# Kernel tuning notes

Measured on AMD Instinct MI355X. Metric: run time of the kernel, lower is better.

## Reference

```python
import jax, jax.numpy as jnp
import numpy as np

B, OBS, H, N = 16384, 512, 1024, 9

def setup_inputs() -> dict:
    key = jax.random.key(0)
    ks = jax.random.split(key, 12)
    s = 0.02
    return {
        "obs": jax.random.normal(ks[0], (B, OBS), jnp.float32),
        "agent_positions": jax.random.normal(ks[1], (B, N, 3), jnp.float32),
        "W1": jax.random.normal(ks[2], (OBS, H), jnp.float32) * s,
        "b1": jnp.zeros((H,), jnp.float32),
        "W2": jax.random.normal(ks[3], (H, H), jnp.float32) * s,
        "b2": jnp.zeros((H,), jnp.float32),
        "Wc1": jax.random.normal(ks[4], (H, H // 2), jnp.float32) * s,
        "bc1": jnp.zeros((H // 2,), jnp.float32),
        "Wc2": jax.random.normal(ks[5], (H // 2, 1), jnp.float32) * s,
        "bc2": jnp.zeros((1,), jnp.float32),
        "Wt1": jax.random.normal(ks[6], (H, H // 2), jnp.float32) * s,
        "bt1": jnp.zeros((H // 2,), jnp.float32),
        "Wt2": jax.random.normal(ks[7], (H // 2, 1), jnp.float32) * s,
        "bt2": jnp.zeros((1,), jnp.float32),
        "Wk1": jax.random.normal(ks[8], (2 * H, H), jnp.float32) * s,
        "bk1": jnp.zeros((H,), jnp.float32),
        "Wk2": jax.random.normal(ks[9], (H, 1), jnp.float32) * s,
        "bk2": jnp.zeros((1,), jnp.float32),
    }


def reference(obs, agent_positions, W1, b1, W2, b2, Wc1, bc1, Wc2, bc2,
              Wt1, bt1, Wt2, bt2, Wk1, bk1, Wk2, bk2):
    # global features: Linear->ReLU->Linear->ReLU
    g = jax.nn.relu(obs @ W1 + b1)
    g = jax.nn.relu(g @ W2 + b2)  # [B, H]

    # Each per-agent head is applied to the SAME g in the original loop,
    # so one pass + broadcast is mathematically identical.
    cov = jax.nn.sigmoid(jax.nn.relu(g @ Wc1 + bc1) @ Wc2 + bc2)  # [B,1]
    trk = jax.nn.sigmoid(jax.nn.relu(g @ Wt1 + bt1) @ Wt2 + bt2)  # [B,1]
    coop_in = jnp.concatenate([g, g], axis=-1)                    # [B,2H]
    coop = jax.nn.sigmoid(jax.nn.relu(coop_in @ Wk1 + bk1) @ Wk2 + bk2)  # [B,1]
    # mean over 8 identical cooperation scores == the score itself

    coverage = jnp.broadcast_to(cov, (cov.shape[0], N))      # [B, N]
    tracking = jnp.broadcast_to(trk, (trk.shape[0], N))      # [B, N]
    cooperation = jnp.broadcast_to(coop, (coop.shape[0], N)) # [B, N]
    return (coverage, tracking, cooperation)
```

## Files before the change

### kernel.cpp

```cpp
#include <hip/hip_runtime.h>
#include <hip/hip_bf16.h>

#define B_ROWS 16384
#define OBS_D  512
#define H_D    1024
#define N_AG   9

typedef __attribute__((ext_vector_type(8))) short short8;
typedef __attribute__((ext_vector_type(4))) float floatx4;

__device__ __forceinline__ unsigned short f_to_bf_raw(float f) {
  union { float f; unsigned u; } c; c.f = f;
  unsigned u = c.u;
  u = u + 0x7FFF + ((u >> 16) & 1);
  return (unsigned short)(u >> 16);
}

__device__ __forceinline__ size_t frag_off(int n, int k, int KT32) {
  const int ft = (n >> 4) * KT32 + (k >> 5);
  const int ln = (n & 15) | (((k >> 3) & 3) << 4);
  return ((size_t)ft * 64 + ln) * 8 + (k & 7);
}

__global__ __launch_bounds__(256) void prep_all(
    const float* __restrict__ obs,
    const float* __restrict__ W1, const float* __restrict__ W2,
    const float* __restrict__ Wc1, const float* __restrict__ Wt1,
    const float* __restrict__ Wk1,
    const float* __restrict__ bc1, const float* __restrict__ bt1,
    const float* __restrict__ bk1,
    const float* __restrict__ Wc2, const float* __restrict__ Wt2,
    const float* __restrict__ Wk2,
    unsigned short* __restrict__ obs_bf,
    unsigned short* __restrict__ W1f, unsigned short* __restrict__ W2f,
    unsigned short* __restrict__ WHf,
    float* __restrict__ bias2048, float* __restrict__ w2cat) {
  __shared__ float t[32][33];
  const int bx  = blockIdx.x;
  const int tid = threadIdx.x;

  if (bx < 4096) {
    int i = (bx * 256 + tid) * 8;
    float4 a = *(const float4*)(obs + i);
    float4 b = *(const float4*)(obs + i + 4);
    short8 o;
    o[0] = (short)f_to_bf_raw(a.x); o[1] = (short)f_to_bf_raw(a.y);
    o[2] = (short)f_to_bf_raw(a.z); o[3] = (short)f_to_bf_raw(a.w);
    o[4] = (short)f_to_bf_raw(b.x); o[5] = (short)f_to_bf_raw(b.y);
    o[6] = (short)f_to_bf_raw(b.z); o[7] = (short)f_to_bf_raw(b.w);
    *(short8*)(obs_bf + i) = o;
    return;
  }

  const int tx = tid & 31;
  const int ty = tid >> 5;

  if (bx < 4608) {
    const int tt = bx - 4096;
    const int k0 = (tt & 15) * 32;
    const int n0 = (tt >> 4) * 32;
#pragma unroll
    for (int i = ty; i < 32; i += 8)
      t[i][tx] = W1[(size_t)(k0 + i) * 1024 + n0 + tx];
    __syncthreads();
#pragma unroll
    for (int i = ty; i < 32; i += 8)
      W1f[frag_off(n0 + i, k0 + tx, 16)] = f_to_bf_raw(t[tx][i]);
    return;
  }

  if (bx < 5632) {
    const int tt = bx - 4608;
    const int k0 = (tt & 31) * 32;
    const int n0 = (tt >> 5) * 32;
#pragma unroll
    for (int i = ty; i < 32; i += 8)
      t[i][tx] = W2[(size_t)(k0 + i) * 1024 + n0 + tx];
    __syncthreads();
#pragma unroll
    for (int i = ty; i < 32; i += 8)
      W2f[frag_off(n0 + i, k0 + tx, 32)] = f_to_bf_raw(t[tx][i]);
    return;
  }

  if (bx < 7680) {
    const int tt = bx - 5632;
    const int k0 = (tt & 31) * 32;
    const int n0 = (tt >> 5) * 32;
#pragma unroll
    for (int i = ty; i < 32; i += 8) {
      const int n = n0 + tx;
      float v;
      if (n0 < 512)
        v = Wc1[(size_t)(k0 + i) * 512 + n];
      else if (n0 < 1024)
        v = Wt1[(size_t)(k0 + i) * 512 + (n - 512)];
      else
        v = Wk1[(size_t)(k0 + i) * 1024 + (n - 1024)]
          + Wk1[(size_t)(k0 + i + 1024) * 1024 + (n - 1024)];
      t[i][tx] = v;
    }
    __syncthreads();
#pragma unroll
    for (int i = ty; i < 32; i += 8)
      WHf[frag_off(n0 + i, k0 + tx, 32)] = f_to_bf_raw(t[tx][i]);
    return;
  }

  {
    int n = (bx - 7680) * 256 + tid;
    float b, w;
    if (n < 512)       { b = bc1[n];        w = Wc2[n]; }
    else if (n < 1024) { b = bt1[n - 512];  w = Wt2[n - 512]; }
    else               { b = bk1[n - 1024]; w = Wk2[n - 1024]; }
    bias2048[n] = b;
    w2cat[n] = w;
  }
}

#define GLD_LDS(gp, lp)                                                        \
  __builtin_amdgcn_global_load_lds(                                            \
      (const __attribute__((address_space(1))) void*)(gp),                     \
      (__attribute__((address_space(3))) void*)(lp), 16, 0, 0)

#define GEMM_CORE_V9(ACC_DECL)                                                 \
  __shared__ __align__(16) unsigned short As[3][128 * 64];          \
  const int tid  = threadIdx.x;                                                \
  const int lane = tid & 63;                                                   \
  const int wave = tid >> 6;                                                   \
  const int m0 = blockIdx.x * 128;                                             \
  const int n0 = blockIdx.y * 128;                                             \
  const int wm = (wave & 1) * 64;                                              \
  const int wn = (wave >> 1) * 64;                                             \
  const int fr = lane & 15;                                                    \
  const int fq = lane >> 4;                                                    \
  ACC_DECL;                                                                    \
  constexpr int KT   = K >> 6;                      \
  constexpr int KT32 = K >> 5;                      \
  const size_t rowb = (size_t)K * 2;                                           \
  const int srow8  = lane >> 3;                   \
  const int schunk = (lane & 7) ^ srow8;          \
  const char* gA = (const char*)A + (size_t)(m0 + wave * 32 + srow8) * rowb    \
                   + schunk * 16;                                              \
  char* lA = (char*)&As[0][0] + wave * 4096 + lane * 16;                       \
  const unsigned short* gB =                                                   \
      Bf + ((size_t)(((n0 + wn) >> 4) * KT32) * 64 + lane) * 8;                \
  const int fsA = (wm + fr) * 128;                                             \
  const int sl0 = ((fq)     ^ (fr & 7)) * 16;                                  \
  const int sl1 = ((4 + fq) ^ (fr & 7)) * 16;                                  \
  short8 FbP[2][2][4];                                                         \
                  \
  _Pragma("unroll")                                                            \
  for (int j = 0; j < 4; ++j)                                                  \
    GLD_LDS(gA + (size_t)j * 8 * rowb, lA + j * 1024);                         \
  _Pragma("unroll")                                                            \
  for (int j = 0; j < 4; ++j)                                                  \
    GLD_LDS(gA + 128 + (size_t)j * 8 * rowb,                                   \
            (char*)&As[1][0] + wave * 4096 + lane * 16 + j * 1024);            \
  _Pragma("unroll")                                                            \
  for (int s = 0; s < 2; ++s)                                                  \
    _Pragma("unroll")                                                          \
    for (int ni = 0; ni < 4; ++ni)                                             \
      FbP[0][s][ni] = *(const short8*)(gB + ((size_t)ni * KT32 + s) * 512);    \
  _Pragma("unroll")                                                            \
  for (int k = 0; k < KT; ++k) {           \
    __syncthreads();            \
    if (k + 2 < KT) {                                                          \
      char* d = (char*)&As[(k + 2) % 3][0] + wave * 4096 + lane * 16;          \
      const char* g = gA + (size_t)(k + 2) * 128;                              \
      _Pragma("unroll")                                                        \
      for (int j = 0; j < 4; ++j)                                              \
        GLD_LDS(g + (size_t)j * 8 * rowb, d + j * 1024);                       \
    }                                                                          \
    if (k + 1 < KT) {                                                          \
      _Pragma("unroll")                                                        \
      for (int s = 0; s < 2; ++s)                                              \
        _Pragma("unroll")                                                      \
        for (int ni = 0; ni < 4; ++ni)                                         \
          FbP[(k + 1) & 1][s][ni] = *(const short8*)                           \
              (gB + ((size_t)ni * KT32 + 2 * (k + 1) + s) * 512);              \
    }                                                                          \
    const char* bA = (const char*)&As[k % 3][0];                               \
    short8 Fa0[4], Fa1[4];                                                     \
    _Pragma("unroll")                                                          \
    for (int mi = 0; mi < 4; ++mi)                                             \
      Fa0[mi] = *(const short8*)(bA + fsA + mi * 2048 + sl0);                  \
    _Pragma("unroll")                                                          \
    for (int mi = 0; mi < 4; ++mi)                                             \
      Fa1[mi] = *(const short8*)(bA + fsA + mi * 2048 + sl1);                  \
    _Pragma("unroll")                                                          \
    for (int mi = 0; mi < 4; ++mi)                                             \
      _Pragma("unroll")                                                        \
      for (int ni = 0; ni < 4; ++ni)                                           \
        acc[mi][ni] = __builtin_amdgcn_mfma_f32_16x16x32_bf16(                 \
            Fa0[mi], FbP[k & 1][0][ni], acc[mi][ni], 0, 0, 0);                 \
    _Pragma("unroll")                                                          \
    for (int mi = 0; mi < 4; ++mi)                                             \
      _Pragma("unroll")                                                        \
      for (int ni = 0; ni < 4; ++ni)                                           \
        acc[mi][ni] = __builtin_amdgcn_mfma_f32_16x16x32_bf16(                 \
            Fa1[mi], FbP[k & 1][1][ni], acc[mi][ni], 0, 0, 0);                 \
  }

#define ACC_INIT                                                               \
  floatx4 acc[4][4];                                                           \
  _Pragma("unroll")                                                            \
  for (int i = 0; i < 4; ++i)                                                  \
    _Pragma("unroll")                                                          \
    for (int j = 0; j < 4; ++j) acc[i][j] = (floatx4){0.f, 0.f, 0.f, 0.f}

template <int K>
__global__ __launch_bounds__(256, 2) void gemm_bias_relu(
    const unsigned short* __restrict__ A,
    const unsigned short* __restrict__ Bf,
    const float* __restrict__ bias,
    unsigned short* __restrict__ C,
    int M, int N) {
  GEMM_CORE_V9(ACC_INIT)

#pragma unroll
  for (int ni = 0; ni < 4; ++ni) {
    const int gn = n0 + wn + ni * 16 + fr;
    const float bv = bias[gn];
#pragma unroll
    for (int mi = 0; mi < 4; ++mi) {
#pragma unroll
      for (int r = 0; r < 4; ++r) {
        const int gm = m0 + wm + mi * 16 + fq * 4 + r;
        float v = acc[mi][ni][r] + bv;
        v = v > 0.f ? v : 0.f;
        C[(size_t)gm * N + gn] = f_to_bf_raw(v);
      }
    }
  }
}

template <int K>
__global__ __launch_bounds__(256, 2) void gemm_heads_fused(
    const unsigned short* __restrict__ A,
    const unsigned short* __restrict__ Bf,
    const float* __restrict__ bias,
    const float* __restrict__ w2,
    float* __restrict__ part,
    int M, int N) {
  GEMM_CORE_V9(ACC_INIT)

  const int j = blockIdx.y * 2 + (wave >> 1);
  float w2v[4], bv[4];
#pragma unroll
  for (int ni = 0; ni < 4; ++ni) {
    const int gn = n0 + wn + ni * 16 + fr;
    w2v[ni] = w2[gn];
    bv[ni]  = bias[gn];
  }
#pragma unroll
  for (int mi = 0; mi < 4; ++mi) {
#pragma unroll
    for (int r = 0; r < 4; ++r) {
      float p = 0.f;
#pragma unroll
      for (int ni = 0; ni < 4; ++ni) {
        float v = acc[mi][ni][r] + bv[ni];
        v = v > 0.f ? v : 0.f;
        p += v * w2v[ni];
      }
      p += __shfl_xor(p, 1);
      p += __shfl_xor(p, 2);
      p += __shfl_xor(p, 4);
      p += __shfl_xor(p, 8);
      if (fr == 0) {
        const int gm = m0 + wm + mi * 16 + fq * 4 + r;
        part[(size_t)j * B_ROWS + gm] = p;
      }
    }
  }
}

__global__ __launch_bounds__(256) void final_out(
    const float* __restrict__ part,
    const float* __restrict__ bc2, const float* __restrict__ bt2,
    const float* __restrict__ bk2, float* __restrict__ out) {
  const int row = blockIdx.x * 256 + threadIdx.x;
  float sc = 0.f, st = 0.f, sk = 0.f;
#pragma unroll
  for (int j = 0; j < 8; ++j)  sc += part[(size_t)j * B_ROWS + row];
#pragma unroll
  for (int j = 8; j < 16; ++j) st += part[(size_t)j * B_ROWS + row];
#pragma unroll
  for (int j = 16; j < 32; ++j) sk += part[(size_t)j * B_ROWS + row];
  const float cv = 1.f / (1.f + expf(-(sc + bc2[0])));
  const float tv = 1.f / (1.f + expf(-(st + bt2[0])));
  const float kv = 1.f / (1.f + expf(-(sk + bk2[0])));
  float* o0 = out + (size_t)row * N_AG;
  float* o1 = out + (size_t)(B_ROWS + row) * N_AG;
  float* o2 = out + (size_t)(2 * B_ROWS + row) * N_AG;
#pragma unroll
  for (int a = 0; a < N_AG; ++a) { o0[a] = cv; o1[a] = tv; o2[a] = kv; }
}

extern "C" void kernel_launch(void* const* d_in, const int* in_sizes, int n_in,
                              void* d_out, int out_size, void* d_ws, size_t ws_size,
                              hipStream_t stream) {
  const float* obs = (const float*)d_in[0];
  const float* W1  = (const float*)d_in[2];
  const float* b1  = (const float*)d_in[3];
  const float* W2  = (const float*)d_in[4];
  const float* b2  = (const float*)d_in[5];
  const float* Wc1 = (const float*)d_in[6];
  const float* bc1 = (const float*)d_in[7];
  const float* Wc2 = (const float*)d_in[8];
  const float* bc2 = (const float*)d_in[9];
  const float* Wt1 = (const float*)d_in[10];
  const float* bt1 = (const float*)d_in[11];
  const float* Wt2 = (const float*)d_in[12];
  const float* bt2 = (const float*)d_in[13];
  const float* Wk1 = (const float*)d_in[14];
  const float* bk1 = (const float*)d_in[15];
  const float* Wk2 = (const float*)d_in[16];
  const float* bk2 = (const float*)d_in[17];
  float* out = (float*)d_out;

  char* ws = (char*)d_ws;
  const size_t MB = 1024 * 1024;
  const size_t FULL_NEED = 70 * MB + 16 * 1024;

  unsigned short *obs_bf, *W1f, *W2f, *WHf, *G1, *G;
  float *bias2048, *w2cat, *PART;
  const bool full = (ws_size == 0) || (ws_size >= FULL_NEED);

  if (full) {
    obs_bf   = (unsigned short*)(ws + 0);
    W1f      = (unsigned short*)(ws + 16 * MB);
    G        = (unsigned short*)(ws + 0);
    G1       = (unsigned short*)(ws + 32 * MB);
    PART     = (float*)(ws + 32 * MB);
    W2f      = (unsigned short*)(ws + 64 * MB);
    WHf      = (unsigned short*)(ws + 66 * MB);
    bias2048 = (float*)(ws + 70 * MB);
    w2cat    = (float*)(ws + 70 * MB + 8 * 1024);
  } else {
    obs_bf   = (unsigned short*)(ws + 0);
    G1       = (unsigned short*)(ws + 16 * MB);
    G        = (unsigned short*)(ws + 32 * MB);
    W1f      = (unsigned short*)(ws + 48 * MB);
    W2f      = (unsigned short*)(ws + 49 * MB);
    WHf      = (unsigned short*)(ws + 51 * MB);
    bias2048 = (float*)(ws + 55 * MB);
    w2cat    = (float*)(ws + 55 * MB + 8 * 1024);
    PART     = (float*)(ws + 55 * MB + 16 * 1024);
  }

  prep_all<<<7688, 256, 0, stream>>>(obs, W1, W2, Wc1, Wt1, Wk1,
                                     bc1, bt1, bk1, Wc2, Wt2, Wk2,
                                     obs_bf, W1f, W2f, WHf, bias2048, w2cat);

  if (full) {
    gemm_bias_relu<512><<<dim3(128, 8), 256, 0, stream>>>(
        obs_bf, W1f, b1, G1, B_ROWS, 1024);
    gemm_bias_relu<1024><<<dim3(128, 8), 256, 0, stream>>>(
        G1, W2f, b2, G, B_ROWS, 1024);
    gemm_heads_fused<1024><<<dim3(128, 16), 256, 0, stream>>>(
        G, WHf, bias2048, w2cat, PART, B_ROWS, 2048);
  } else {
    for (int h = 0; h < 2; ++h) {
      const size_t ro = (size_t)h * 8192;
      gemm_bias_relu<512><<<dim3(64, 8), 256, 0, stream>>>(
          obs_bf + ro * 512, W1f, b1, G1, 8192, 1024);
      gemm_bias_relu<1024><<<dim3(64, 8), 256, 0, stream>>>(
          G1, W2f, b2, G, 8192, 1024);
      gemm_heads_fused<1024><<<dim3(64, 16), 256, 0, stream>>>(
          G, WHf, bias2048, w2cat, PART + ro, 8192, 2048);
    }
  }

  final_out<<<B_ROWS / 256, 256, 0, stream>>>(PART, bc2, bt2, bk2, out);
}
```

Baseline: 246.6 us.

## Enlarge GEMM tiles to 256x256 with 8 waves and pinned barrier scheduling

Grows each GEMM block tile from 128x128 to 256x256, with 512 threads and each wave holding a 128x64 accumulator tile. This raises arithmetic intensity per loaded fragment. The K loop is restructured: A-fragment LDS reads and B-fragment global prefetches are interleaved with MFMA groups, split by sched_barrier-pinned s_barriers, with s_setprio raised around the MFMA bursts and explicit vmcnt/lgkmcnt waits replacing __syncthreads. The trade-offs are much higher register pressure (128 accumulator floats per lane) and a 96KB LDS triple buffer that limits occupancy. The grid also gets fewer blocks, which may hurt load balance across CUs.

```diff
diff --git a/kernel.cpp b/kernel.cpp
--- a/kernel.cpp
+++ b/kernel.cpp
@@ -123,14 +123,21 @@
       (const __attribute__((address_space(1))) void*)(gp),                     \
       (__attribute__((address_space(3))) void*)(lp), 16, 0, 0)
 
-#define GEMM_CORE_V9(ACC_DECL)                                                 \
-  __shared__ __align__(16) unsigned short As[3][128 * 64];          \
+#define SBAR_PINNED()                                                          \
+  __builtin_amdgcn_sched_barrier(0);                                           \
+  __builtin_amdgcn_s_barrier();                                                \
+  __builtin_amdgcn_sched_barrier(0)
+
+#define MFMA_BF16(a, b, c) __builtin_amdgcn_mfma_f32_16x16x32_bf16(a, b, c, 0, 0, 0)
+
+#define GEMM_CORE_V10(ACC_DECL)                                                \
+  __shared__ __align__(16) unsigned short As[3][256 * 64];          \
   const int tid  = threadIdx.x;                                                \
   const int lane = tid & 63;                                                   \
-  const int wave = tid >> 6;                                                   \
-  const int m0 = blockIdx.x * 128;                                             \
-  const int n0 = blockIdx.y * 128;                                             \
-  const int wm = (wave & 1) * 64;                                              \
+  const int wave = tid >> 6;                                         \
+  const int m0 = blockIdx.x * 256;                                             \
+  const int n0 = blockIdx.y * 256;                                             \
+  const int wm = (wave & 1) * 128;                  \
   const int wn = (wave >> 1) * 64;                                             \
   const int fr = lane & 15;                                                    \
   const int fq = lane >> 4;                                                    \
@@ -142,88 +149,98 @@
   const int schunk = (lane & 7) ^ srow8;          \
   const char* gA = (const char*)A + (size_t)(m0 + wave * 32 + srow8) * rowb    \
                    + schunk * 16;                                              \
-  char* lA = (char*)&As[0][0] + wave * 4096 + lane * 16;                       \
   const unsigned short* gB =                                                   \
       Bf + ((size_t)(((n0 + wn) >> 4) * KT32) * 64 + lane) * 8;                \
   const int fsA = (wm + fr) * 128;                                             \
   const int sl0 = ((fq)     ^ (fr & 7)) * 16;                                  \
   const int sl1 = ((4 + fq) ^ (fr & 7)) * 16;                                  \
   short8 FbP[2][2][4];                                                         \
-                  \
+        \
+        \
   _Pragma("unroll")                                                            \
   for (int j = 0; j < 4; ++j)                                                  \
-    GLD_LDS(gA + (size_t)j * 8 * rowb, lA + j * 1024);                         \
+    GLD_LDS(gA + (size_t)j * 8 * rowb,                                         \
+            (char*)&As[0][0] + wave * 4096 + lane * 16 + j * 1024);            \
+  __builtin_amdgcn_sched_barrier(0);                                           \
   _Pragma("unroll")                                                            \
   for (int j = 0; j < 4; ++j)                                                  \
     GLD_LDS(gA + 128 + (size_t)j * 8 * rowb,                                   \
             (char*)&As[1][0] + wave * 4096 + lane * 16 + j * 1024);            \
+  __builtin_amdgcn_sched_barrier(0);                                           \
   _Pragma("unroll")                                                            \
   for (int s = 0; s < 2; ++s)                                                  \
     _Pragma("unroll")                                                          \
     for (int ni = 0; ni < 4; ++ni)                                             \
       FbP[0][s][ni] = *(const short8*)(gB + ((size_t)ni * KT32 + s) * 512);    \
-  _Pragma("unroll")                                                            \
-  for (int k = 0; k < KT; ++k) {           \
-    __syncthreads();            \
-    if (k + 2 < KT) {                                                          \
-      char* d = (char*)&As[(k + 2) % 3][0] + wave * 4096 + lane * 16;          \
-      const char* g = gA + (size_t)(k + 2) * 128;                              \
+  __builtin_amdgcn_sched_barrier(0);                                           \
+  asm volatile("s_waitcnt vmcnt(12)" ::: "memory");        \
+  __builtin_amdgcn_s_barrier();                                                \
+  __builtin_amdgcn_sched_barrier(0);                                           \
+  _Pragma("unroll")                                                            \
+  for (int t = 0; t < KT; ++t) {           \
+    if (t + 2 < KT) {                      \
+      char* d = (char*)&As[(t + 2) % 3][0] + wave * 4096 + lane * 16;          \
+      const char* g = gA + (size_t)(t + 2) * 128;                              \
       _Pragma("unroll")                                                        \
       for (int j = 0; j < 4; ++j)                                              \
         GLD_LDS(g + (size_t)j * 8 * rowb, d + j * 1024);                       \
     }                                                                          \
-    if (k + 1 < KT) {                                                          \
+    const char* bA = (const char*)&As[t % 3][0];                               \
+    _Pragma("unroll")                                                          \
+    for (int p = 0; p < 4; ++p) {           \
+      short8 Fa00 = *(const short8*)(bA + fsA + (2 * p) * 2048     + sl0);     \
+      short8 Fa01 = *(const short8*)(bA + fsA + (2 * p) * 2048     + sl1);     \
+      short8 Fa10 = *(const short8*)(bA + fsA + (2 * p + 1) * 2048 + sl0);     \
+      short8 Fa11 = *(const short8*)(bA + fsA + (2 * p + 1) * 2048 + sl1);     \
+      if (t + 1 < KT) {                           \
+        FbP[(t + 1) & 1][0][p] = *(const short8*)                              \
+            (gB + ((size_t)p * KT32 + 2 * (t + 1)) * 512);                     \
+        FbP[(t + 1) & 1][1][p] = *(const short8*)                              \
+            (gB + ((size_t)p * KT32 + 2 * (t + 1) + 1) * 512);                 \
+      }                                                                        \
+      SBAR_PINNED();                                                           \
+      __builtin_amdgcn_s_setprio(1);                                           \
       _Pragma("unroll")                                                        \
-      for (int s = 0; s < 2; ++s)                                              \
-        _Pragma("unroll")                                                      \
-        for (int ni = 0; ni < 4; ++ni)                                         \
-          FbP[(k + 1) & 1][s][ni] = *(const short8*)                           \
-              (gB + ((size_t)ni * KT32 + 2 * (k + 1) + s) * 512);              \
+      for (int ni = 0; ni < 4; ++ni) {                                         \
+        acc[2 * p][ni]     = MFMA_BF16(Fa00, FbP[t & 1][0][ni], acc[2 * p][ni]);     \
+        acc[2 * p][ni]     = MFMA_BF16(Fa01, FbP[t & 1][1][ni], acc[2 * p][ni]);     \
+        acc[2 * p + 1][ni] = MFMA_BF16(Fa10, FbP[t & 1][0][ni], acc[2 * p + 1][ni]); \
+        acc[2 * p + 1][ni] = MFMA_BF16(Fa11, FbP[t & 1][1][ni], acc[2 * p + 1][ni]); \
+      }                                                                        \
+      __builtin_amdgcn_s_setprio(0);                                           \
+      if (p < 3) { SBAR_PINNED(); }                                            \
     }                                                                          \
-    const char* bA = (const char*)&As[k % 3][0];                               \
-    short8 Fa0[4], Fa1[4];                                                     \
-    _Pragma("unroll")                                                          \
-    for (int mi = 0; mi < 4; ++mi)                                             \
-      Fa0[mi] = *(const short8*)(bA + fsA + mi * 2048 + sl0);                  \
-    _Pragma("unroll")                                                          \
-    for (int mi = 0; mi < 4; ++mi)                                             \
-      Fa1[mi] = *(const short8*)(bA + fsA + mi * 2048 + sl1);                  \
-    _Pragma("unroll")                                                          \
-    for (int mi = 0; mi < 4; ++mi)                                             \
-      _Pragma("unroll")                                                        \
-      for (int ni = 0; ni < 4; ++ni)                                           \
-        acc[mi][ni] = __builtin_amdgcn_mfma_f32_16x16x32_bf16(                 \
-            Fa0[mi], FbP[k & 1][0][ni], acc[mi][ni], 0, 0, 0);                 \
-    _Pragma("unroll")                                                          \
-    for (int mi = 0; mi < 4; ++mi)                                             \
-      _Pragma("unroll")                                                        \
-      for (int ni = 0; ni < 4; ++ni)                                           \
-        acc[mi][ni] = __builtin_amdgcn_mfma_f32_16x16x32_bf16(                 \
-            Fa1[mi], FbP[k & 1][1][ni], acc[mi][ni], 0, 0, 0);                 \
+          \
+          \
+          \
+    __builtin_amdgcn_sched_barrier(0);                                         \
+    asm volatile("s_waitcnt vmcnt(12) lgkmcnt(0)" ::: "memory");               \
+    __builtin_amdgcn_s_barrier();                                              \
+    __builtin_amdgcn_sched_barrier(0);                                         \
   }
 
 #define ACC_INIT                                                               \
-  floatx4 acc[4][4];                                                           \
-  _Pragma("unroll")                                                            \
-  for (int i = 0; i < 4; ++i)                                                  \
+  floatx4 acc[8][4];                                                           \
+  _Pragma("unroll")                                                            \
+  for (int i = 0; i < 8; ++i)                                                  \
     _Pragma("unroll")                                                          \
     for (int j = 0; j < 4; ++j) acc[i][j] = (floatx4){0.f, 0.f, 0.f, 0.f}
 
 template <int K>
-__global__ __launch_bounds__(256, 2) void gemm_bias_relu(
+__global__ __launch_bounds__(512, 2) void gemm_bias_relu(
     const unsigned short* __restrict__ A,
     const unsigned short* __restrict__ Bf,
     const float* __restrict__ bias,
     unsigned short* __restrict__ C,
     int M, int N) {
-  GEMM_CORE_V9(ACC_INIT)
+  GEMM_CORE_V10(ACC_INIT)
 
 #pragma unroll
   for (int ni = 0; ni < 4; ++ni) {
     const int gn = n0 + wn + ni * 16 + fr;
     const float bv = bias[gn];
 #pragma unroll
-    for (int mi = 0; mi < 4; ++mi) {
+    for (int mi = 0; mi < 8; ++mi) {
 #pragma unroll
       for (int r = 0; r < 4; ++r) {
         const int gm = m0 + wm + mi * 16 + fq * 4 + r;
@@ -236,16 +253,16 @@
 }
 
 template <int K>
-__global__ __launch_bounds__(256, 2) void gemm_heads_fused(
+__global__ __launch_bounds__(512, 2) void gemm_heads_fused(
     const unsigned short* __restrict__ A,
     const unsigned short* __restrict__ Bf,
     const float* __restrict__ bias,
     const float* __restrict__ w2,
     float* __restrict__ part,
     int M, int N) {
-  GEMM_CORE_V9(ACC_INIT)
-
-  const int j = blockIdx.y * 2 + (wave >> 1);
+  GEMM_CORE_V10(ACC_INIT)
+
+  const int j = blockIdx.y * 4 + (wave >> 1);
   float w2v[4], bv[4];
 #pragma unroll
   for (int ni = 0; ni < 4; ++ni) {
@@ -254,7 +271,7 @@
     bv[ni]  = bias[gn];
   }
 #pragma unroll
-  for (int mi = 0; mi < 4; ++mi) {
+  for (int mi = 0; mi < 8; ++mi) {
 #pragma unroll
     for (int r = 0; r < 4; ++r) {
       float p = 0.f;
@@ -355,20 +372,20 @@
                                      obs_bf, W1f, W2f, WHf, bias2048, w2cat);
 
   if (full) {
-    gemm_bias_relu<512><<<dim3(128, 8), 256, 0, stream>>>(
+    gemm_bias_relu<512><<<dim3(64, 4), 512, 0, stream>>>(
         obs_bf, W1f, b1, G1, B_ROWS, 1024);
-    gemm_bias_relu<1024><<<dim3(128, 8), 256, 0, stream>>>(
+    gemm_bias_relu<1024><<<dim3(64, 4), 512, 0, stream>>>(
         G1, W2f, b2, G, B_ROWS, 1024);
-    gemm_heads_fused<1024><<<dim3(128, 16), 256, 0, stream>>>(
+    gemm_heads_fused<1024><<<dim3(64, 8), 512, 0, stream>>>(
         G, WHf, bias2048, w2cat, PART, B_ROWS, 2048);
   } else {
     for (int h = 0; h < 2; ++h) {
       const size_t ro = (size_t)h * 8192;
-      gemm_bias_relu<512><<<dim3(64, 8), 256, 0, stream>>>(
+      gemm_bias_relu<512><<<dim3(32, 4), 512, 0, stream>>>(
           obs_bf + ro * 512, W1f, b1, G1, 8192, 1024);
-      gemm_bias_relu<1024><<<dim3(64, 8), 256, 0, stream>>>(
+      gemm_bias_relu<1024><<<dim3(32, 4), 512, 0, stream>>>(
           G1, W2f, b2, G, 8192, 1024);
-      gemm_heads_fused<1024><<<dim3(64, 16), 256, 0, stream>>>(
+      gemm_heads_fused<1024><<<dim3(32, 8), 512, 0, stream>>>(
           G, WHf, bias2048, w2cat, PART + ro, 8192, 2048);
     }
   }
```

Result: slower. 262.1 us (+6.3%).

## Rewrite heads GEMM with 256x256 tiles, LDS-staged B, and explicit pipelining

Applied to the files above, without the earlier changes.

The fused heads GEMM moves to a new core with 256x256 block tiles and 512 threads (8 waves), each wave computing 128x64. Both A and B are now staged through a 128KB double-buffered LDS region using global_load_lds, and the loop uses explicit vmcnt waits, sched barriers and setprio around the MFMA bursts. The larger tile is meant to raise data reuse and cut global traffic on the biggest GEMM. The cost is more LDS per block (limiting occupancy) and more accumulator registers per wave.

```diff
diff --git a/kernel.cpp b/kernel.cpp
--- a/kernel.cpp
+++ b/kernel.cpp
@@ -122,6 +122,10 @@
   __builtin_amdgcn_global_load_lds(                                            \
       (const __attribute__((address_space(1))) void*)(gp),                     \
       (__attribute__((address_space(3))) void*)(lp), 16, 0, 0)
+
+#define SCB __builtin_amdgcn_sched_barrier(0)
+
+#define MFMA_BF16(a, b, c) __builtin_amdgcn_mfma_f32_16x16x32_bf16(a, b, c, 0, 0, 0)
 
 #define GEMM_CORE_V9(ACC_DECL)                                                 \
   __shared__ __align__(16) unsigned short As[3][128 * 64];          \
@@ -149,7 +153,6 @@
   const int sl0 = ((fq)     ^ (fr & 7)) * 16;                                  \
   const int sl1 = ((4 + fq) ^ (fr & 7)) * 16;                                  \
   short8 FbP[2][2][4];                                                         \
-                  \
   _Pragma("unroll")                                                            \
   for (int j = 0; j < 4; ++j)                                                  \
     GLD_LDS(gA + (size_t)j * 8 * rowb, lA + j * 1024);                         \
@@ -202,10 +205,112 @@
             Fa1[mi], FbP[k & 1][1][ni], acc[mi][ni], 0, 0, 0);                 \
   }
 
-#define ACC_INIT                                                               \
+#define ACC_INIT4                                                              \
   floatx4 acc[4][4];                                                           \
   _Pragma("unroll")                                                            \
   for (int i = 0; i < 4; ++i)                                                  \
+    _Pragma("unroll")                                                          \
+    for (int j = 0; j < 4; ++j) acc[i][j] = (floatx4){0.f, 0.f, 0.f, 0.f}
+
+#define ST_A16(T, kh)                                                          \
+  GLD_LDS(gA0 + (size_t)(T) * 128 + (kh) * 64,                                 \
+          Lds + ((T) & 1) * 65536 + (kh) * 16384 + lA0);                       \
+  GLD_LDS(gA1 + (size_t)(T) * 128 + (kh) * 64,                                 \
+          Lds + ((T) & 1) * 65536 + (kh) * 16384 + lA0 + 8192)
+
+#define ST_B16(T, kh)                                                          \
+  GLD_LDS(gB0 + (size_t)(2 * (T) + (kh)) * 1024,                               \
+          Lds + ((T) & 1) * 65536 + (kh) * 16384 + lB0);                       \
+  GLD_LDS(gB1 + (size_t)(2 * (T) + (kh)) * 1024,                               \
+          Lds + ((T) & 1) * 65536 + (kh) * 16384 + lB0 + 8192)
+
+#define ROW16(mi, FA)                                                          \
+  acc[mi][0] = MFMA_BF16(FA, Fb0v, acc[mi][0]);                                \
+  acc[mi][1] = MFMA_BF16(FA, Fb1v, acc[mi][1]);                                \
+  acc[mi][2] = MFMA_BF16(FA, Fb2v, acc[mi][2]);                                \
+  acc[mi][3] = MFMA_BF16(FA, Fb3v, acc[mi][3])
+
+#define PHASE16(TT, ks, STAGE_STMT, PRE_BAR2)                                  \
+  {                                                                            \
+    const char* pb = Lds + ((TT) & 1) * 65536 + (ks) * 16384;                  \
+    short8 Fa0 = *(const short8*)(pb + faB + 0 * 1024);                        \
+    short8 Fa1 = *(const short8*)(pb + faB + 1 * 1024);                        \
+    short8 Fa2 = *(const short8*)(pb + faB + 2 * 1024);                        \
+    short8 Fa3 = *(const short8*)(pb + faB + 3 * 1024);                        \
+    short8 Fa4 = *(const short8*)(pb + faB + 4 * 1024);                        \
+    short8 Fa5 = *(const short8*)(pb + faB + 5 * 1024);                        \
+    short8 Fa6 = *(const short8*)(pb + faB + 6 * 1024);                        \
+    short8 Fa7 = *(const short8*)(pb + faB + 7 * 1024);                        \
+    short8 Fb0v = *(const short8*)(pb + fbB);                                  \
+    short8 Fb1v = *(const short8*)(pb + fbB + 1024);                           \
+    short8 Fb2v = *(const short8*)(pb + fbB + 2048);                           \
+    short8 Fb3v = *(const short8*)(pb + fbB + 3072);                           \
+    STAGE_STMT;                                                                \
+    SCB; __builtin_amdgcn_s_barrier(); SCB;                                    \
+    __builtin_amdgcn_s_setprio(1);                                             \
+    ROW16(0, Fa0); ROW16(1, Fa1); ROW16(2, Fa2); ROW16(3, Fa3);                \
+    ROW16(4, Fa4); ROW16(5, Fa5); ROW16(6, Fa6); ROW16(7, Fa7);                \
+    __builtin_amdgcn_s_setprio(0);                                             \
+    PRE_BAR2;                                                                  \
+    SCB; __builtin_amdgcn_s_barrier(); SCB;                                    \
+  }
+
+#define GEMM_CORE_V16(ACC_DECL)                                                \
+  __shared__ __align__(16) char Lds[131072];                                   \
+  const int tid  = threadIdx.x;                                                \
+  const int lane = tid & 63;                                                   \
+  const int wave = tid >> 6;                                         \
+  const int m0 = blockIdx.x * 256;                                             \
+  const int n0 = blockIdx.y * 256;                                             \
+  const int wm = (wave & 1) * 128;                  \
+  const int wn = (wave >> 1) * 64;                                             \
+  const int fr = lane & 15;                                                    \
+  const int fq = lane >> 4;                                                    \
+  ACC_DECL;                                                                    \
+  constexpr int KT   = K >> 6;                                                 \
+  constexpr int KT32 = K >> 5;                                                 \
+  const size_t rowb = (size_t)K * 2;                                           \
+  const char* gA0 = (const char*)A                                             \
+      + (size_t)(m0 + wave * 16 + (lane >> 2)) * rowb                          \
+      + (((lane & 3) ^ ((lane >> 3) & 3)) * 16);                               \
+  const char* gA1 = gA0 + (size_t)128 * rowb;                                  \
+  const char* gB0 = (const char*)Bf                                            \
+      + ((size_t)((n0 >> 4) + wave) * KT32) * 1024 + lane * 16;                \
+  const char* gB1 = gB0 + (size_t)8 * KT32 * 1024;                             \
+  const int lA0 = wave * 1024 + lane * 16;                                     \
+  const int lB0 = 32768 + wave * 1024 + lane * 16;                             \
+  const int faB = (wm + fr) * 64 + ((fq ^ ((fr >> 1) & 3)) * 16);              \
+  const int fbB = 32768 + ((wave >> 1) * 4) * 1024 + lane * 16;                \
+               \
+  ST_A16(0, 0); ST_B16(0, 0); ST_A16(0, 1); ST_B16(0, 1);                      \
+  SCB;                                                                         \
+  ST_A16(1, 0); ST_B16(1, 0);                                                  \
+  SCB;                                                                         \
+  asm volatile("s_waitcnt vmcnt(4)" ::: "memory");       \
+  __builtin_amdgcn_s_barrier();                  \
+  SCB;                                                                         \
+  _Pragma("unroll")                                                            \
+  for (int T = 0; T < KT; ++T) {           \
+    PHASE16(T, 0,                                                              \
+            { if (T + 1 < KT) { ST_A16(T + 1, 1); ST_B16(T + 1, 1); } },       \
+            (void)0);                                                          \
+    PHASE16(T, 1,                                                              \
+            { if (T + 2 < KT) { ST_A16(T + 2, 0); ST_B16(T + 2, 0); } },       \
+            if (T + 1 < KT) {                                                  \
+              SCB;                                                             \
+              if (T + 2 < KT) {                                                \
+                asm volatile("s_waitcnt vmcnt(4)" ::: "memory");               \
+              } else {                                                         \
+                asm volatile("s_waitcnt vmcnt(0)" ::: "memory");               \
+              }                                                                \
+              SCB;                                                             \
+            });                                                                \
+  }
+
+#define ACC_INIT8                                                              \
+  floatx4 acc[8][4];                                                           \
+  _Pragma("unroll")                                                            \
+  for (int i = 0; i < 8; ++i)                                                  \
     _Pragma("unroll")                                                          \
     for (int j = 0; j < 4; ++j) acc[i][j] = (floatx4){0.f, 0.f, 0.f, 0.f}
 
@@ -216,7 +321,7 @@
     const float* __restrict__ bias,
     unsigned short* __restrict__ C,
     int M, int N) {
-  GEMM_CORE_V9(ACC_INIT)
+  GEMM_CORE_V9(ACC_INIT4)
 
 #pragma unroll
   for (int ni = 0; ni < 4; ++ni) {
@@ -236,16 +341,16 @@
 }
 
 template <int K>
-__global__ __launch_bounds__(256, 2) void gemm_heads_fused(
+__global__ __launch_bounds__(512, 2) void gemm_heads_fused(
     const unsigned short* __restrict__ A,
     const unsigned short* __restrict__ Bf,
     const float* __restrict__ bias,
     const float* __restrict__ w2,
     float* __restrict__ part,
     int M, int N) {
-  GEMM_CORE_V9(ACC_INIT)
-
-  const int j = blockIdx.y * 2 + (wave >> 1);
+  GEMM_CORE_V16(ACC_INIT8)
+
+  const int j = blockIdx.y * 4 + (wave >> 1);
   float w2v[4], bv[4];
 #pragma unroll
   for (int ni = 0; ni < 4; ++ni) {
@@ -254,7 +359,7 @@
     bv[ni]  = bias[gn];
   }
 #pragma unroll
-  for (int mi = 0; mi < 4; ++mi) {
+  for (int mi = 0; mi < 8; ++mi) {
 #pragma unroll
     for (int r = 0; r < 4; ++r) {
       float p = 0.f;
@@ -359,7 +464,7 @@
         obs_bf, W1f, b1, G1, B_ROWS, 1024);
     gemm_bias_relu<1024><<<dim3(128, 8), 256, 0, stream>>>(
         G1, W2f, b2, G, B_ROWS, 1024);
-    gemm_heads_fused<1024><<<dim3(128, 16), 256, 0, stream>>>(
+    gemm_heads_fused<1024><<<dim3(64, 8), 512, 0, stream>>>(
         G, WHf, bias2048, w2cat, PART, B_ROWS, 2048);
   } else {
     for (int h = 0; h < 2; ++h) {
@@ -368,7 +473,7 @@
           obs_bf + ro * 512, W1f, b1, G1, 8192, 1024);
       gemm_bias_relu<1024><<<dim3(64, 8), 256, 0, stream>>>(
           G1, W2f, b2, G, 8192, 1024);
-      gemm_heads_fused<1024><<<dim3(64, 16), 256, 0, stream>>>(
+      gemm_heads_fused<1024><<<dim3(32, 8), 512, 0, stream>>>(
           G, WHf, bias2048, w2cat, PART + ro, 8192, 2048);
     }
   }
```

Result: no change. 249.7 us (+1.2%).
